# Optimization experiments

Hardware: AMD Instinct MI355X
Metric: run time of the kernel (lower is better)

Reference implementation:

```python
import jax, jax.numpy as jnp
import numpy as np

TEMPERATURE = 0.5


def setup_inputs() -> dict:
    key = jax.random.key(0)
    k1, k2 = jax.random.split(key)
    N, D = 4096, 256
    emb_i = jax.random.normal(k1, (N, D), dtype=jnp.float32)
    emb_j = jax.random.normal(k2, (N, D), dtype=jnp.float32)
    return {"emb_i": emb_i, "emb_j": emb_j, "batch_size": N}


def reference(emb_i, emb_j, batch_size):
    N = batch_size
    # L2-normalize each embedding row (F.normalize eps=1e-12)
    def l2n(x):
        return x / jnp.maximum(jnp.linalg.norm(x, axis=1, keepdims=True), 1e-12)
    reps = jnp.concatenate([l2n(emb_i), l2n(emb_j)], axis=0)  # [2N, D]
    # cosine similarity of normalized vectors == dot product
    logits = (reps @ reps.T) / TEMPERATURE                    # [2N, 2N]
    twoN = 2 * N
    # denominator excludes only the self term k != i (stable logsumexp)
    diag_mask = jnp.eye(twoN, dtype=bool)
    masked = jnp.where(diag_mask, -jnp.inf, logits)
    log_denom = jax.nn.logsumexp(masked, axis=1)              # [2N]
    # positive pair for row i is (i+N) mod 2N
    idx = jnp.arange(twoN)
    pos = logits[idx, (idx + N) % twoN]                       # [2N]
    # loss = 1/(2N) * sum_i -log(exp(pos_i)/denom_i)
    return jnp.mean(log_denom - pos)
```

## Files before the change

### kernel.cpp

```cpp
#include <hip/hip_runtime.h>

typedef short short8 __attribute__((ext_vector_type(8)));
typedef float f32x4  __attribute__((ext_vector_type(4)));

#define TWO_N 8192
#define NHALF 4096
#define DDIM  256

__device__ __forceinline__ float b2f(unsigned short u) {
    return __uint_as_float(((unsigned int)u) << 16);
}
__device__ __forceinline__ unsigned short f2b(float f) {
    unsigned int u = __float_as_uint(f);
    u += 0x7fffu + ((u >> 16) & 1u);
    return (unsigned short)(u >> 16);
}

__device__ __forceinline__ int probe_is_f32(const void* p, int lane) {
    unsigned int u = ((const unsigned int*)p)[lane];
    float lowv = __uint_as_float(u << 16);
    int crazy = !(fabsf(lowv) <= 1024.0f);
    return __ballot(crazy) != 0ull;
}

typedef __attribute__((address_space(1))) const unsigned int guint_t;
typedef __attribute__((address_space(3))) unsigned int luint_t;
__device__ __forceinline__ void gl_lds16(const unsigned short* g, unsigned short* l) {
    __builtin_amdgcn_global_load_lds((guint_t*)(const void*)g, (luint_t*)(void*)l, 16, 0, 0);
}

__device__ __forceinline__ void ast(float* p, float v) {
    __hip_atomic_store(p, v, __ATOMIC_RELAXED, __HIP_MEMORY_SCOPE_AGENT);
}
__device__ __forceinline__ float ald(const float* p) {
    return __hip_atomic_load(p, __ATOMIC_RELAXED, __HIP_MEMORY_SCOPE_AGENT);
}

__global__ __launch_bounds__(256) void k_norm(const void* __restrict__ ei,
                                              const void* __restrict__ ej,
                                              unsigned short* __restrict__ reps,
                                              unsigned int* __restrict__ ctr) {
    if (blockIdx.x == 0 && threadIdx.x == 0)
        __hip_atomic_store(ctr, 0u, __ATOMIC_RELAXED, __HIP_MEMORY_SCOPE_AGENT);

    int row  = (blockIdx.x * 256 + threadIdx.x) >> 6;
    int lane = threadIdx.x & 63;
    int isf  = probe_is_f32(ei, lane);
    int first = (row < NHALF);
    int r     = first ? row : row - NHALF;
    float x0, x1, x2, x3;
    if (isf) {
        const float* s = (first ? (const float*)ei : (const float*)ej) + (size_t)r * DDIM;
        float4 v = ((const float4*)s)[lane];
        x0 = v.x; x1 = v.y; x2 = v.z; x3 = v.w;
    } else {
        const unsigned short* s =
            (first ? (const unsigned short*)ei : (const unsigned short*)ej) + (size_t)r * DDIM;
        ushort4 v = ((const ushort4*)s)[lane];
        x0 = b2f(v.x); x1 = b2f(v.y); x2 = b2f(v.z); x3 = b2f(v.w);
    }
    float ss = x0 * x0 + x1 * x1 + x2 * x2 + x3 * x3;
    for (int off = 32; off > 0; off >>= 1) ss += __shfl_xor(ss, off);
    float inv = 1.0f / fmaxf(sqrtf(ss), 1e-12f);
    ushort4 o;
    o.x = f2b(x0 * inv); o.y = f2b(x1 * inv);
    o.z = f2b(x2 * inv); o.w = f2b(x3 * inv);
    ((ushort4*)(reps + (size_t)row * DDIM))[lane] = o;
}

__global__ __launch_bounds__(256, 4) void k_main(const unsigned short* __restrict__ R,
                                                 float* __restrict__ S_part,
                                                 float* __restrict__ pos) {
    __shared__ __align__(16) unsigned short As[128 * 64];
    __shared__ __align__(16) unsigned short Bs[128 * 64];

    int b = (int)blockIdx.x;
    int rb = (int)((129.0f - sqrtf(16641.0f - 8.0f * (float)b)) * 0.5f);
    if (rb > 63) rb = 63;
    while ((129 * (rb + 1) - (rb + 1) * (rb + 1)) / 2 <= b) ++rb;
    while ((129 * rb - rb * rb) / 2 > b) --rb;
    int cb = rb + (b - (129 * rb - rb * rb) / 2);

    const int tid  = threadIdx.x;
    const int wave = tid >> 6;
    const int lane = tid & 63;
    const int quad = lane >> 4;
    const int l16  = lane & 15;
    const int wr   = (wave >> 1) * 64;
    const int wc   = (wave & 1) * 64;
    const int r8   = lane >> 3;
    const int c8   = (lane & 7) ^ r8;

    f32x4 acc[4][4];
#pragma unroll
    for (int r = 0; r < 4; ++r)
#pragma unroll
        for (int c = 0; c < 4; ++c) {
            acc[r][c][0] = 0.0f; acc[r][c][1] = 0.0f;
            acc[r][c][2] = 0.0f; acc[r][c][3] = 0.0f;
        }

    for (int kc = 0; kc < 4; ++kc) {
        __syncthreads();
#pragma unroll
        for (int t = 0; t < 4; ++t) {
            int u = wave * 4 + t;
            const unsigned short* ga =
                R + (size_t)(rb * 128 + u * 8 + r8) * DDIM + kc * 64 + c8 * 8;
            const unsigned short* gb =
                R + (size_t)(cb * 128 + u * 8 + r8) * DDIM + kc * 64 + c8 * 8;
            gl_lds16(ga, &As[u * 512]);
            gl_lds16(gb, &Bs[u * 512]);
        }
        __syncthreads();

#pragma unroll
        for (int kk = 0; kk < 2; ++kk) {
            short8 afr[4], bfr[4];
            int q = kk * 4 + quad;
            int sl = q ^ (l16 & 7);
#pragma unroll
            for (int r = 0; r < 4; ++r)
                afr[r] = *(const short8*)(&As[(wr + r * 16 + l16) * 64 + sl * 8]);
#pragma unroll
            for (int c = 0; c < 4; ++c)
                bfr[c] = *(const short8*)(&Bs[(wc + c * 16 + l16) * 64 + sl * 8]);
#pragma unroll
            for (int r = 0; r < 4; ++r)
#pragma unroll
                for (int c = 0; c < 4; ++c)
                    acc[r][c] = __builtin_amdgcn_mfma_f32_16x16x32_bf16(
                        afr[r], bfr[c], acc[r][c], 0, 0, 0);
        }
    }

    float col_acc[4] = {0.0f, 0.0f, 0.0f, 0.0f};
#pragma unroll
    for (int r = 0; r < 4; ++r)
#pragma unroll
        for (int j = 0; j < 4; ++j) {
            float s = 0.0f;
#pragma unroll
            for (int c = 0; c < 4; ++c) {
                float e = __expf(fmaf(acc[r][c][j], 2.0f, -2.0f));
                s += e;
                col_acc[c] += e;
            }
            s += __shfl_xor(s, 1);
            s += __shfl_xor(s, 2);
            s += __shfl_xor(s, 4);
            s += __shfl_xor(s, 8);
            if (l16 == 0) {
                int row = rb * 128 + wr + r * 16 + quad * 4 + j;
                S_part[(size_t)(2 * cb + (wave & 1)) * TWO_N + row] = s;
            }
        }
    if (rb != cb) {
#pragma unroll
        for (int c = 0; c < 4; ++c) {
            float s = col_acc[c];
            s += __shfl_xor(s, 16);
            s += __shfl_xor(s, 32);
            if (lane < 16) {
                int row = cb * 128 + wc + c * 16 + lane;
                S_part[(size_t)(2 * rb + (wave >> 1)) * TWO_N + row] = s;
            }
        }
    }
    if (cb == rb + 32 && wr == wc) {
#pragma unroll
        for (int r = 0; r < 4; ++r)
#pragma unroll
            for (int j = 0; j < 4; ++j)
                if (quad * 4 + j == l16)
                    pos[rb * 128 + wr + r * 16 + l16] = 2.0f * acc[r][r][j];
    }
}

__global__ __launch_bounds__(256) void k_rows(const float* __restrict__ S_part,
                                              const float* __restrict__ pos,
                                              float* __restrict__ part_blk,
                                              unsigned int* __restrict__ ctr,
                                              unsigned int* __restrict__ out) {
    __shared__ float red[256];
    __shared__ float red2[4];
    __shared__ unsigned int sdone;
    int tid = threadIdx.x;
    int rr  = tid & 63;
    int cg  = tid >> 6;
    int row = blockIdx.x * 64 + rr;
    float s = 0.0f;
#pragma unroll 8
    for (int c = cg * 32; c < cg * 32 + 32; ++c)
        s += S_part[(size_t)c * TWO_N + row];
    red[tid] = s;
    __syncthreads();
    if (tid < 64) {
        float total = red[tid] + red[tid + 64] + red[tid + 128] + red[tid + 192];
        float p = (row < NHALF) ? pos[row] : pos[row - NHALF];
        float part = 2.0f + logf(total - 1.0f) - p;
        for (int off = 32; off > 0; off >>= 1) part += __shfl_xor(part, off);
        if (tid == 0) ast(&part_blk[blockIdx.x], part);
    }
    __syncthreads();
    if (tid == 0)
        sdone = __hip_atomic_fetch_add(ctr, 1u, __ATOMIC_RELAXED,
                                       __HIP_MEMORY_SCOPE_AGENT);
    __syncthreads();
    if (sdone == 127u) {
        float v = (tid < 128) ? ald(&part_blk[tid]) : 0.0f;
        for (int off = 32; off > 0; off >>= 1) v += __shfl_xor(v, off);
        if ((tid & 63) == 0) red2[tid >> 6] = v;
        __syncthreads();
        if (tid == 0) {
            float L = (red2[0] + red2[1] + red2[2] + red2[3]) / 8192.0f;
            unsigned int bb = (unsigned int)f2b(L);
            out[0] = (bb << 16) | bb;
        }
    }
}

extern "C" void kernel_launch(void* const* d_in, const int* in_sizes, int n_in,
                              void* d_out, int out_size, void* d_ws, size_t ws_size,
                              hipStream_t stream) {
    (void)in_sizes; (void)n_in; (void)out_size; (void)ws_size;
    const void* ei = d_in[0];
    const void* ej = d_in[1];
    char* ws = (char*)d_ws;

    float*          pos      = (float*)(ws);
    float*          part_blk = (float*)(ws + 16384);
    unsigned int*   ctr      = (unsigned int*)(ws + 17408);
    unsigned short* reps     = (unsigned short*)(ws + 49152);
    float*          S_part   = (float*)(ws + 4243456);

    k_norm<<<2048, 256, 0, stream>>>(ei, ej, reps, ctr);
    k_main<<<2080, 256, 0, stream>>>(reps, S_part, pos);
    k_rows<<<128,  256, 0, stream>>>(S_part, pos, part_blk, ctr, (unsigned int*)d_out);
}
```

Measured before the change: 98.88 us.

## Give each wave a private LDS tile to drop block-wide barriers

Each wave now loads its own 64-row A and B slices into a private LDS region (64 KB per block total) and waits only on its own vmcnt/lgkmcnt, instead of sharing 128-row tiles behind two __syncthreads per k-chunk. This removes block-level synchronisation stalls. In exchange each A/B slice is loaded twice per block, which doubles global/L2 traffic and LDS footprint. The min-blocks launch bound is dropped, so occupancy likely falls.

```diff
diff --git a/kernel.cpp b/kernel.cpp
--- a/kernel.cpp
+++ b/kernel.cpp
@@ -68,11 +68,10 @@
     ((ushort4*)(reps + (size_t)row * DDIM))[lane] = o;
 }
 
-__global__ __launch_bounds__(256, 4) void k_main(const unsigned short* __restrict__ R,
-                                                 float* __restrict__ S_part,
-                                                 float* __restrict__ pos) {
-    __shared__ __align__(16) unsigned short As[128 * 64];
-    __shared__ __align__(16) unsigned short Bs[128 * 64];
+__global__ __launch_bounds__(256) void k_main(const unsigned short* __restrict__ R,
+                                              float* __restrict__ S_part,
+                                              float* __restrict__ pos) {
+    __shared__ __align__(16) unsigned short WS[4][8192];
 
     int b = (int)blockIdx.x;
     int rb = (int)((129.0f - sqrtf(16641.0f - 8.0f * (float)b)) * 0.5f);
@@ -91,6 +90,11 @@
     const int r8   = lane >> 3;
     const int c8   = (lane & 7) ^ r8;
 
+    unsigned short* Wa = &WS[wave][0];
+    unsigned short* Wb = &WS[wave][4096];
+    const unsigned short* Ga = R + (size_t)(rb * 128 + wr) * DDIM;
+    const unsigned short* Gb = R + (size_t)(cb * 128 + wc) * DDIM;
+
     f32x4 acc[4][4];
 #pragma unroll
     for (int r = 0; r < 4; ++r)
@@ -101,30 +105,28 @@
         }
 
     for (int kc = 0; kc < 4; ++kc) {
-        __syncthreads();
-#pragma unroll
-        for (int t = 0; t < 4; ++t) {
-            int u = wave * 4 + t;
-            const unsigned short* ga =
-                R + (size_t)(rb * 128 + u * 8 + r8) * DDIM + kc * 64 + c8 * 8;
-            const unsigned short* gb =
-                R + (size_t)(cb * 128 + u * 8 + r8) * DDIM + kc * 64 + c8 * 8;
-            gl_lds16(ga, &As[u * 512]);
-            gl_lds16(gb, &Bs[u * 512]);
-        }
-        __syncthreads();
+        if (kc)
+            asm volatile("s_waitcnt lgkmcnt(0)" ::: "memory");
+#pragma unroll
+        for (int u = 0; u < 8; ++u) {
+            gl_lds16(Ga + (size_t)(u * 8 + r8) * DDIM + kc * 64 + c8 * 8,
+                     &Wa[u * 512]);
+            gl_lds16(Gb + (size_t)(u * 8 + r8) * DDIM + kc * 64 + c8 * 8,
+                     &Wb[u * 512]);
+        }
+        asm volatile("s_waitcnt vmcnt(0)" ::: "memory");
 
 #pragma unroll
         for (int kk = 0; kk < 2; ++kk) {
             short8 afr[4], bfr[4];
-            int q = kk * 4 + quad;
+            int q  = kk * 4 + quad;
             int sl = q ^ (l16 & 7);
 #pragma unroll
             for (int r = 0; r < 4; ++r)
-                afr[r] = *(const short8*)(&As[(wr + r * 16 + l16) * 64 + sl * 8]);
+                afr[r] = *(const short8*)(&Wa[(r * 16 + l16) * 64 + sl * 8]);
 #pragma unroll
             for (int c = 0; c < 4; ++c)
-                bfr[c] = *(const short8*)(&Bs[(wc + c * 16 + l16) * 64 + sl * 8]);
+                bfr[c] = *(const short8*)(&Wb[(c * 16 + l16) * 64 + sl * 8]);
 #pragma unroll
             for (int r = 0; r < 4; ++r)
 #pragma unroll
```

After: 108.8 us. 10.1% more time.
